# Performance work log

Hardware: AMD Instinct MI355X
Metric: run time of the kernel (lower is better)

The kernel has to match this reference:

```python
import jax, jax.numpy as jnp
import numpy as np

B, S, E, H, T = 2, 1024, 1024, 16, 32
D = E // H  # head_dim = 64
EPS = 1e-12
SCALE = float(np.sqrt(T) / np.sqrt(D))  # sqrt(num_templates) * 1/sqrt(head_dim)


def _apply_rope(q, k):
    # q, k: [B, S, H, D] float32 (source casts to float for RoPE)
    d = q.shape[-1]
    s = q.shape[1]
    inv_freq = 1.0 / (10000.0 ** (jnp.arange(0, d, 2, dtype=jnp.float32) / d))
    ang = jnp.arange(s, dtype=jnp.float32)[:, None] * inv_freq[None, :]  # [S, D/2]
    cis = jnp.exp(1j * ang)[None, :, None, :]  # [1, S, 1, D/2] complex64

    def rot(v):
        vc = v.reshape(v.shape[:-1] + (d // 2, 2))
        vc = jax.lax.complex(vc[..., 0], vc[..., 1]) * cis
        return jnp.stack([jnp.real(vc), jnp.imag(vc)], axis=-1).reshape(v.shape)

    return rot(q), rot(k)


def _l2norm(v):
    # F.normalize(v, dim=-1): v / max(||v||, eps)
    n = jnp.sqrt(jnp.sum(v * v, axis=-1, keepdims=True))
    return v / jnp.maximum(n, EPS)


def _forward(x, Wq, Wk, Wv, Wo, templates, bind_proj):
    b, s, e = x.shape
    h, d = H, D
    q = (x @ Wq.T).reshape(b, s, h, d)
    k = (x @ Wk.T).reshape(b, s, h, d)
    v = (x @ Wv.T).reshape(b, s, h, d)
    q, k = _apply_rope(q, k)
    q = q.transpose(0, 2, 1, 3)  # [B,H,S,D]
    k = k.transpose(0, 2, 1, 3)
    v = v.transpose(0, 2, 1, 3)

    tpl = _l2norm(templates)  # [H,T,D]
    # forward rfft uses norm='ortho' in the source
    q_freq = jnp.fft.rfft(q, axis=-1, norm='ortho')  # [B,H,S,F], F=D//2+1
    k_freq = jnp.fft.rfft(k, axis=-1, norm='ortho')
    t_conj = jnp.conj(jnp.fft.rfft(tpl, axis=-1, norm='ortho'))[None, :, None, :, :]  # [1,H,1,T,F]

    # NOTE: irfft in the source uses the DEFAULT 'backward' norm (asymmetric with
    # the ortho rfft) -- reproduce that exactly.
    q_bind = jnp.fft.irfft(q_freq[:, :, :, None, :] * t_conj, n=d, axis=-1)  # [B,H,S,T,D]
    k_bind = jnp.fft.irfft(k_freq[:, :, :, None, :] * t_conj, n=d, axis=-1)

    proj = bind_proj[None, :, None, None, :]  # [1,H,1,1,D]
    q_sig = _l2norm(jnp.sum(q_bind * proj, axis=-1))  # [B,H,S,T]
    k_sig = _l2norm(jnp.sum(k_bind * proj, axis=-1))

    scores = jnp.einsum('bhqt,bhkt->bhqk', q_sig, k_sig) * SCALE  # [B,H,S,S]
    attn = jax.nn.softmax(scores, axis=-1)  # dropout is identity in eval mode
    out = jnp.einsum('bhqk,bhkd->bqhd', attn, v).reshape(b, s, e)
    return out @ Wo.T


def setup_inputs() -> dict:
    key = jax.random.key(0)
    ks = jax.random.split(key, 7)
    lim = 1.0 / np.sqrt(E)
    x = jax.random.normal(ks[0], (B, S, E), jnp.float32)
    Wq = jax.random.uniform(ks[1], (E, E), jnp.float32, -lim, lim)
    Wk = jax.random.uniform(ks[2], (E, E), jnp.float32, -lim, lim)
    Wv = jax.random.uniform(ks[3], (E, E), jnp.float32, -lim, lim)
    Wo = jax.random.uniform(ks[4], (E, E), jnp.float32, -lim, lim)
    templates = jax.random.normal(ks[5], (H, T, D), jnp.float32)
    bind_proj = jax.random.normal(ks[6], (H, D), jnp.float32) * 0.02
    return {"x": x, "Wq": Wq, "Wk": Wk, "Wv": Wv, "Wo": Wo,
            "templates": templates, "bind_proj": bind_proj}


def reference(x, Wq, Wk, Wv, Wo, templates, bind_proj):
    return _forward(x, Wq, Wk, Wv, Wo, templates, bind_proj)
```

## Files before the change

kernel.cpp:

```cpp
#include <hip/hip_runtime.h>
#include <math.h>

#define S_ 1024
#define T_ 32
#define SCALE_F 0.7071067811865476f

typedef unsigned int uint;
typedef unsigned short ushort;
typedef __bf16 bf16x8 __attribute__((ext_vector_type(8)));
typedef float f32x16 __attribute__((ext_vector_type(16)));

union FragU { uint4 q; bf16x8 v; };

#define MFMA(a, b, c) __builtin_amdgcn_mfma_f32_32x32x16_bf16((a), (b), (c), 0, 0, 0)

__device__ __forceinline__ uint rne16(float f) {
  uint u = __builtin_bit_cast(uint, f);
  u += 0x7fffu + ((u >> 16) & 1u);
  return u >> 16;
}

__device__ __forceinline__ float bf2f(ushort u) {
  return __builtin_bit_cast(float, ((uint)u) << 16);
}

__device__ __forceinline__ void split8a(const float* f, uint4& hi, uint4& lo) {
  uint h[8], m[8];
#pragma unroll
  for (int i = 0; i < 8; ++i) {
    uint u = __builtin_bit_cast(uint, f[i]);
    h[i] = u >> 16;
    float fh = __builtin_bit_cast(float, u & 0xffff0000u);
    m[i] = __builtin_bit_cast(uint, f[i] - fh) >> 16;
  }
  hi = make_uint4(h[0] | (h[1] << 16), h[2] | (h[3] << 16),
                  h[4] | (h[5] << 16), h[6] | (h[7] << 16));
  lo = make_uint4(m[0] | (m[1] << 16), m[2] | (m[3] << 16),
                  m[4] | (m[5] << 16), m[6] | (m[7] << 16));
}

__device__ __forceinline__ uint4 rne8(const float4& A, const float4& B) {
  float f[8] = {A.x, A.y, A.z, A.w, B.x, B.y, B.z, B.w};
  uint h[8];
#pragma unroll
  for (int i = 0; i < 8; ++i) h[i] = rne16(f[i]);
  return make_uint4(h[0] | (h[1] << 16), h[2] | (h[3] << 16),
                    h[4] | (h[5] << 16), h[6] | (h[7] << 16));
}

__global__ __launch_bounds__(256) void k_prep(
    const float* __restrict__ X, const float* __restrict__ Wq,
    const float* __restrict__ Wk, const float* __restrict__ Wv,
    const float* __restrict__ Wo, const float* __restrict__ tpl,
    const float* __restrict__ proj, ushort* __restrict__ Xb,
    ushort* __restrict__ Wqb, ushort* __restrict__ Wkb,
    ushort* __restrict__ Wvb, ushort* __restrict__ Wob,
    float* __restrict__ cs, ushort* __restrict__ Ahh,
    ushort* __restrict__ Ahl) {
  const int bid = blockIdx.x;
  const int tid = threadIdx.x;

  if (bid < 3072) {
    int i = bid * 256 + tid;
    const float* src;
    ushort* dst;
    int j;
    if (i < 262144)      { src = X;  dst = Xb;  j = i; }
    else if (i < 393216) { src = Wq; dst = Wqb; j = i - 262144; }
    else if (i < 524288) { src = Wk; dst = Wkb; j = i - 393216; }
    else if (i < 655360) { src = Wv; dst = Wvb; j = i - 524288; }
    else                 { src = Wo; dst = Wob; j = i - 655360; }
    float4 a = *reinterpret_cast<const float4*>(src + j * 8);
    float4 b = *reinterpret_cast<const float4*>(src + j * 8 + 4);
    *reinterpret_cast<uint4*>(dst + j * 8) = rne8(a, b);
    return;
  }

  if (bid < 3200) {
    int j = (bid - 3072) * 256 + tid;
    int s = j >> 5, p = j & 31;
    float invf = powf(10000.0f, (-2.0f * p) / 64.0f);
    float sn, c;
    sincosf((float)s * invf, &sn, &c);
    cs[s * 64 + 2 * p] = c;
    cs[s * 64 + 2 * p + 1] = sn;
    return;
  }

  {
    __shared__ float tn[4][64];
    int wid = tid >> 6, lane = tid & 63;
    int ht = (bid - 3200) * 4 + wid;
    int h = ht >> 5;
    float tv = tpl[ht * 64 + lane];
    float ss = tv * tv;
#pragma unroll
    for (int off2 = 1; off2 < 64; off2 <<= 1) ss += __shfl_xor(ss, off2);
    float rn = 1.0f / fmaxf(sqrtf(ss), 1e-12f);
    tn[wid][lane] = tv * rn;
    __syncthreads();
    float acc = 0.f;
#pragma unroll
    for (int j2 = 0; j2 < 64; ++j2)
      acc += proj[h * 64 + j2] * tn[wid][(lane - j2) & 63];
    float v = acc * 0.125f;
    uint u = __builtin_bit_cast(uint, v);
    uint hi = u >> 16;
    float fh = __builtin_bit_cast(float, u & 0xffff0000u);
    uint lo = __builtin_bit_cast(uint, v - fh) >> 16;
    Ahh[ht * 64 + lane] = (ushort)hi;
    Ahl[ht * 64 + lane] = (ushort)lo;
  }
}

__global__ __launch_bounds__(256) void k_qkv(
    const ushort* __restrict__ Xb,
    const ushort* __restrict__ Wqb, const ushort* __restrict__ Wkb,
    const ushort* __restrict__ Wvb,
    const ushort* __restrict__ Ahh, const ushort* __restrict__ Ahl,
    const float* __restrict__ cs,
    ushort* __restrict__ Qs, ushort* __restrict__ Ks,
    ushort* __restrict__ Vt) {
  __shared__ __align__(16) char smem[34816];

  const int z = blockIdx.z;
  const ushort* Wm = (z == 0) ? Wqb : (z == 1) ? Wkb : Wvb;
  const int m0 = blockIdx.y * 128;
  const int n0 = blockIdx.x * 64;
  const int h = blockIdx.x;

  const int tid = threadIdx.x;
  const int l = tid & 63;
  const int wid = tid >> 6;
  const int wr = wid >> 1, wc = wid & 1;
  const int l31 = l & 31, lhi = l >> 5;

  const int sr = tid >> 2;
  const int sc = tid & 3;

  const int offA0 = (sr) * 64 + ((sc ^ ((sr >> 1) & 3)) << 4);
  const int offA1 = (sr + 64) * 64 + ((sc ^ (((sr + 64) >> 1) & 3)) << 4);
  const int offB = 8192 + sr * 64 + ((sc ^ ((sr >> 1) & 3)) << 4);

  const ushort* apsrc0 = Xb + (size_t)(m0 + sr) * 1024 + sc * 8;
  const ushort* apsrc1 = Xb + (size_t)(m0 + sr + 64) * 1024 + sc * 8;
  const ushort* bpsrc = Wm + (size_t)(n0 + sr) * 1024 + sc * 8;

  f32x16 acc0 = 0.0f, acc1 = 0.0f;

  {
    *reinterpret_cast<uint4*>(smem + offA0) =
        *reinterpret_cast<const uint4*>(apsrc0);
    *reinterpret_cast<uint4*>(smem + offA1) =
        *reinterpret_cast<const uint4*>(apsrc1);
    *reinterpret_cast<uint4*>(smem + offB) =
        *reinterpret_cast<const uint4*>(bpsrc);
  }
  uint4 ra0 = *reinterpret_cast<const uint4*>(apsrc0 + 32);
  uint4 ra1 = *reinterpret_cast<const uint4*>(apsrc1 + 32);
  uint4 rb = *reinterpret_cast<const uint4*>(bpsrc + 32);
  __syncthreads();

  int cur = 0;
#pragma unroll 4
  for (int t = 0; t < 32; ++t) {
    uint4 na0, na1, nb;
    if (t < 30) {
      const int kn = (t + 2) * 32;
      na0 = *reinterpret_cast<const uint4*>(apsrc0 + kn);
      na1 = *reinterpret_cast<const uint4*>(apsrc1 + kn);
      nb = *reinterpret_cast<const uint4*>(bpsrc + kn);
    }

    const char* base = smem + cur * 12288;
#pragma unroll
    for (int kst = 0; kst < 2; ++kst) {
      FragU ah0, ah1, bh;
      {
        int row = wr * 64 + l31;
        int cc = (kst * 2 + lhi) ^ ((row >> 1) & 3);
        ah0.q = *reinterpret_cast<const uint4*>(base + row * 64 + cc * 16);
      }
      {
        int row = wr * 64 + 32 + l31;
        int cc = (kst * 2 + lhi) ^ ((row >> 1) & 3);
        ah1.q = *reinterpret_cast<const uint4*>(base + row * 64 + cc * 16);
      }
      {
        int brow = wc * 32 + l31;
        int bcc = (kst * 2 + lhi) ^ ((brow >> 1) & 3);
        bh.q = *reinterpret_cast<const uint4*>(base + 8192 + brow * 64 + bcc * 16);
      }
      acc0 = MFMA(ah0.v, bh.v, acc0);
      acc1 = MFMA(ah1.v, bh.v, acc1);
    }

    if (t < 31) {
      char* dst = smem + (cur ^ 1) * 12288;
      *reinterpret_cast<uint4*>(dst + offA0) = ra0;
      *reinterpret_cast<uint4*>(dst + offA1) = ra1;
      *reinterpret_cast<uint4*>(dst + offB) = rb;
      __syncthreads();
      cur ^= 1;
      if (t < 30) { ra0 = na0; ra1 = na1; rb = nb; }
    }
  }

  if (z == 2) {
    int d = wc * 32 + l31;
#pragma unroll
    for (int fm = 0; fm < 2; ++fm) {
      const f32x16& a = fm ? acc1 : acc0;
#pragma unroll
      for (int j = 0; j < 16; ++j) {
        int rl = fm * 32 + (j & 3) + ((j >> 2) & 3) * 8 + 4 * lhi;
        int m = m0 + wr * 64 + rl;
        int b = m >> 10, s = m & 1023;
        Vt[((size_t)((b * 16 + h) * 64 + d)) * 1024 + s] = (ushort)rne16(a[j]);
      }
    }
    return;
  }

  ushort* Sig = (z == 0) ? Qs : Ks;
  float* dmp = reinterpret_cast<float*>(smem);
  __syncthreads();
#pragma unroll
  for (int fm = 0; fm < 2; ++fm) {
    const f32x16& a = fm ? acc1 : acc0;
#pragma unroll
    for (int j = 0; j < 16; ++j) {
      int rl = fm * 32 + (j & 3) + ((j >> 2) & 3) * 8 + 4 * lhi;
      dmp[(wr * 64 + rl) * 68 + wc * 32 + l31] = a[j];
    }
  }
  __syncthreads();

  int srow = wr * 64 + wc * 32 + l31;
  int sq = (m0 + srow) & 1023;
  f32x16 sacc = 0.0f;
#pragma unroll
  for (int kst = 0; kst < 4; ++kst) {
    const float* dp = &dmp[srow * 68 + kst * 16 + lhi * 8];
    float4 x0 = *reinterpret_cast<const float4*>(dp);
    float4 x1 = *reinterpret_cast<const float4*>(dp + 4);
    const float* cp = &cs[sq * 64 + kst * 16 + lhi * 8];
    float4 c0 = *reinterpret_cast<const float4*>(cp);
    float4 c1 = *reinterpret_cast<const float4*>(cp + 4);
    float r[8];
    r[0] = x0.x * c0.x - x0.y * c0.y;
    r[1] = x0.x * c0.y + x0.y * c0.x;
    r[2] = x0.z * c0.z - x0.w * c0.w;
    r[3] = x0.z * c0.w + x0.w * c0.z;
    r[4] = x1.x * c1.x - x1.y * c1.y;
    r[5] = x1.x * c1.y + x1.y * c1.x;
    r[6] = x1.z * c1.z - x1.w * c1.w;
    r[7] = x1.z * c1.w + x1.w * c1.z;
    FragU ah, al;
    split8a(r, ah.q, al.q);
    size_t boff = ((size_t)(h * 32 + l31) * 64 + kst * 16 + lhi * 8);
    FragU bh, bl;
    bh.q = *reinterpret_cast<const uint4*>(Ahh + boff);
    bl.q = *reinterpret_cast<const uint4*>(Ahl + boff);
    sacc = MFMA(al.v, bh.v, sacc);
    sacc = MFMA(ah.v, bl.v, sacc);
    sacc = MFMA(ah.v, bh.v, sacc);
  }
#pragma unroll
  for (int j = 0; j < 16; ++j) {
    float v = sacc[j];
    float ss = v * v;
    ss += __shfl_xor(ss, 1);
    ss += __shfl_xor(ss, 2);
    ss += __shfl_xor(ss, 4);
    ss += __shfl_xor(ss, 8);
    ss += __shfl_xor(ss, 16);
    float rn = 1.0f / fmaxf(sqrtf(ss), 1e-12f);
    int rl = (j & 3) + ((j >> 2) & 3) * 8 + 4 * lhi;
    int m = m0 + wr * 64 + wc * 32 + rl;
    int bb = m >> 10, s2 = m & 1023;
    Sig[(((size_t)(bb * 16 + h)) * 1024 + s2) * 32 + l31] =
        (ushort)rne16(v * rn);
  }
}

__global__ __launch_bounds__(128) void k_attn(const ushort* __restrict__ Qs,
                                              const ushort* __restrict__ Ks,
                                              const ushort* __restrict__ Vt,
                                              ushort* __restrict__ Po,
                                              float* __restrict__ Pd) {
  __shared__ ushort plds[2][32][68];

  const int tid = threadIdx.x;
  const int l = tid & 63;
  const int wid = tid >> 6;
  const int l31 = l & 31, lhi = l >> 5;
  const int bh = blockIdx.y;
  const int z = blockIdx.z;
  const int q0 = blockIdx.x * 64 + wid * 32;

  FragU aq0, aq1;
  {
    const ushort* qp = Qs + ((size_t)bh * 1024 + q0 + l31) * 32 + lhi * 8;
    aq0.q = *reinterpret_cast<const uint4*>(qp);
    aq1.q = *reinterpret_cast<const uint4*>(qp + 16);
  }

  const ushort* kbase = Ks + (size_t)bh * 1024 * 32;
  const ushort* vbase = Vt + (size_t)bh * 64 * 1024;

  f32x16 oacc0 = 0.0f, oacc1 = 0.0f;
  float pden[16];
#pragma unroll
  for (int r = 0; r < 16; ++r) pden[r] = 0.f;

  const int ktBeg = z * 4;
  FragU kc00, kc01, kc10, kc11;
  {
    const ushort* kp0 = kbase + (size_t)(ktBeg * 64 + l31) * 32 + lhi * 8;
    const ushort* kp1 = kbase + (size_t)(ktBeg * 64 + 32 + l31) * 32 + lhi * 8;
    kc00.q = *reinterpret_cast<const uint4*>(kp0);
    kc01.q = *reinterpret_cast<const uint4*>(kp0 + 16);
    kc10.q = *reinterpret_cast<const uint4*>(kp1);
    kc11.q = *reinterpret_cast<const uint4*>(kp1 + 16);
  }

#pragma unroll
  for (int ki = 0; ki < 4; ++ki) {
    const int kt = ktBeg + ki;
    const int k0 = kt * 64;

    FragU vv00, vv01, vv10, vv11, vv20, vv21, vv30, vv31;
    {
      const ushort* vp = vbase + (size_t)l31 * 1024 + k0 + lhi * 8;
      vv00.q = *reinterpret_cast<const uint4*>(vp);
      vv01.q = *reinterpret_cast<const uint4*>(vp + 32 * 1024);
      vv10.q = *reinterpret_cast<const uint4*>(vp + 16);
      vv11.q = *reinterpret_cast<const uint4*>(vp + 16 + 32 * 1024);
      vv20.q = *reinterpret_cast<const uint4*>(vp + 32);
      vv21.q = *reinterpret_cast<const uint4*>(vp + 32 + 32 * 1024);
      vv30.q = *reinterpret_cast<const uint4*>(vp + 48);
      vv31.q = *reinterpret_cast<const uint4*>(vp + 48 + 32 * 1024);
    }

    f32x16 sacc0 = 0.0f, sacc1 = 0.0f;
    sacc0 = MFMA(aq0.v, kc00.v, sacc0);
    sacc0 = MFMA(aq1.v, kc01.v, sacc0);
    sacc1 = MFMA(aq0.v, kc10.v, sacc1);
    sacc1 = MFMA(aq1.v, kc11.v, sacc1);

    FragU kn00, kn01, kn10, kn11;
    if (ki < 3) {
      const ushort* kp0 = kbase + (size_t)((kt + 1) * 64 + l31) * 32 + lhi * 8;
      const ushort* kp1 =
          kbase + (size_t)((kt + 1) * 64 + 32 + l31) * 32 + lhi * 8;
      kn00.q = *reinterpret_cast<const uint4*>(kp0);
      kn01.q = *reinterpret_cast<const uint4*>(kp0 + 16);
      kn10.q = *reinterpret_cast<const uint4*>(kp1);
      kn11.q = *reinterpret_cast<const uint4*>(kp1 + 16);
    }

#pragma unroll
    for (int r = 0; r < 16; ++r) {
      float e0 = __expf(sacc0[r] * SCALE_F);
      float e1 = __expf(sacc1[r] * SCALE_F);
      pden[r] += e0 + e1;
      int q = (r & 3) + ((r >> 2) << 3) + 4 * lhi;
      plds[wid][q][l31] = (ushort)rne16(e0);
      plds[wid][q][32 + l31] = (ushort)rne16(e1);
    }
    __builtin_amdgcn_wave_barrier();

#pragma unroll
    for (int kst = 0; kst < 4; ++kst) {
      FragU ap;
      const ushort* pp = &plds[wid][l31][kst * 16 + lhi * 8];
      uint2 plo = *reinterpret_cast<const uint2*>(pp);
      uint2 phi = *reinterpret_cast<const uint2*>(pp + 4);
      ap.q = make_uint4(plo.x, plo.y, phi.x, phi.y);
      const FragU& b0 = (kst == 0) ? vv00 : (kst == 1) ? vv10 : (kst == 2) ? vv20 : vv30;
      const FragU& b1 = (kst == 0) ? vv01 : (kst == 1) ? vv11 : (kst == 2) ? vv21 : vv31;
      oacc0 = MFMA(ap.v, b0.v, oacc0);
      oacc1 = MFMA(ap.v, b1.v, oacc1);
    }

    if (ki < 3) { kc00 = kn00; kc01 = kn01; kc10 = kn10; kc11 = kn11; }
  }

#pragma unroll
  for (int r = 0; r < 16; ++r) {
    float s = pden[r];
    s += __shfl_xor(s, 1);
    s += __shfl_xor(s, 2);
    s += __shfl_xor(s, 4);
    s += __shfl_xor(s, 8);
    s += __shfl_xor(s, 16);
    pden[r] = s;
  }

  const size_t zb = (size_t)z * 32 + bh;
#pragma unroll
  for (int r = 0; r < 16; ++r) {
    int q = q0 + (r & 3) + ((r >> 2) << 3) + 4 * lhi;
    size_t row = zb * 1024 + q;
    Po[row * 64 + l31] = (ushort)rne16(oacc0[r]);
    Po[row * 64 + 32 + l31] = (ushort)rne16(oacc1[r]);
    if (l31 == 0) Pd[row] = pden[r];
  }
}

__global__ __launch_bounds__(256) void k_attnred(const ushort* __restrict__ Po,
                                                 const float* __restrict__ Pd,
                                                 ushort* __restrict__ O) {
  int idx = blockIdx.x * 4 + (threadIdx.x >> 6);
  int d = threadIdx.x & 63;
  float den = 0.f, val = 0.f;
#pragma unroll
  for (int zc = 0; zc < 4; ++zc) {
    size_t row = (size_t)zc * 32768 + idx;
    den += Pd[row];
    val += bf2f(Po[row * 64 + d]);
  }
  int bh = idx >> 10, q = idx & 1023;
  int b = bh >> 4, h = bh & 15;
  O[((size_t)(b * 1024 + q)) * 1024 + h * 64 + d] = (ushort)rne16(val / den);
}

__global__ __launch_bounds__(128) void k_attn_mono(const ushort* __restrict__ Qs,
                                                   const ushort* __restrict__ Ks,
                                                   const ushort* __restrict__ Vt,
                                                   ushort* __restrict__ O) {
  __shared__ ushort plds[2][32][68];

  const int tid = threadIdx.x;
  const int l = tid & 63;
  const int wid = tid >> 6;
  const int l31 = l & 31, lhi = l >> 5;
  const int bh = blockIdx.y;
  const int q0 = blockIdx.x * 64 + wid * 32;

  FragU aq0, aq1;
  {
    const ushort* qp = Qs + ((size_t)bh * 1024 + q0 + l31) * 32 + lhi * 8;
    aq0.q = *reinterpret_cast<const uint4*>(qp);
    aq1.q = *reinterpret_cast<const uint4*>(qp + 16);
  }

  const ushort* kbase = Ks + (size_t)bh * 1024 * 32;
  const ushort* vbase = Vt + (size_t)bh * 64 * 1024;

  f32x16 oacc0 = 0.0f, oacc1 = 0.0f;
  float pden[16];
#pragma unroll
  for (int r = 0; r < 16; ++r) pden[r] = 0.f;

  for (int kt = 0; kt < 16; ++kt) {
    const int k0 = kt * 64;
    f32x16 sacc[2];
    sacc[0] = 0.0f;
    sacc[1] = 0.0f;
#pragma unroll
    for (int nt = 0; nt < 2; ++nt) {
      const ushort* kp = kbase + (size_t)(k0 + nt * 32 + l31) * 32 + lhi * 8;
      FragU b0, b1;
      b0.q = *reinterpret_cast<const uint4*>(kp);
      b1.q = *reinterpret_cast<const uint4*>(kp + 16);
      sacc[nt] = MFMA(aq0.v, b0.v, sacc[nt]);
      sacc[nt] = MFMA(aq1.v, b1.v, sacc[nt]);
    }
#pragma unroll
    for (int nt = 0; nt < 2; ++nt) {
#pragma unroll
      for (int r = 0; r < 16; ++r) {
        float e = __expf(sacc[nt][r] * SCALE_F);
        pden[r] += e;
        int q = (r & 3) + ((r >> 2) << 3) + 4 * lhi;
        plds[wid][q][nt * 32 + l31] = (ushort)rne16(e);
      }
    }
    __builtin_amdgcn_wave_barrier();
#pragma unroll
    for (int kst = 0; kst < 4; ++kst) {
      FragU ap;
      const ushort* pp = &plds[wid][l31][kst * 16 + lhi * 8];
      uint2 plo = *reinterpret_cast<const uint2*>(pp);
      uint2 phi = *reinterpret_cast<const uint2*>(pp + 4);
      ap.q = make_uint4(plo.x, plo.y, phi.x, phi.y);
      FragU bv0, bv1;
      const ushort* vp0 = vbase + (size_t)l31 * 1024 + k0 + kst * 16 + lhi * 8;
      bv0.q = *reinterpret_cast<const uint4*>(vp0);
      bv1.q = *reinterpret_cast<const uint4*>(vp0 + 32 * 1024);
      oacc0 = MFMA(ap.v, bv0.v, oacc0);
      oacc1 = MFMA(ap.v, bv1.v, oacc1);
    }
  }

#pragma unroll
  for (int r = 0; r < 16; ++r) {
    float s = pden[r];
    s += __shfl_xor(s, 1);
    s += __shfl_xor(s, 2);
    s += __shfl_xor(s, 4);
    s += __shfl_xor(s, 8);
    s += __shfl_xor(s, 16);
    pden[r] = 1.0f / s;
  }

  const int b = bh >> 4, h = bh & 15;
#pragma unroll
  for (int r = 0; r < 16; ++r) {
    int q = q0 + (r & 3) + ((r >> 2) << 3) + 4 * lhi;
    size_t row = ((size_t)b * 1024 + q) * 1024 + h * 64;
    O[row + l31] = (ushort)rne16(oacc0[r] * pden[r]);
    O[row + 32 + l31] = (ushort)rne16(oacc1[r] * pden[r]);
  }
}

__global__ __launch_bounds__(256) void k_final(const ushort* __restrict__ Xb,
                                               const ushort* __restrict__ Wb,
                                               float* __restrict__ Y) {
  __shared__ __align__(16) char smem[16384];

  const int m0 = blockIdx.y * 64;
  const int n0 = blockIdx.x * 64;
  const int tid = threadIdx.x;
  const int l = tid & 63;
  const int wid = tid >> 6;
  const int wr = wid >> 1, wc = wid & 1;
  const int l31 = l & 31, lhi = l >> 5;
  const int sr = tid >> 2;
  const int sc = tid & 3;

  const int offA = sr * 64 + ((sc ^ ((sr >> 1) & 3)) << 4);
  const int offB = 4096 + offA;
  const ushort* apsrc = Xb + (size_t)(m0 + sr) * 1024 + sc * 8;
  const ushort* bpsrc = Wb + (size_t)(n0 + sr) * 1024 + sc * 8;

  f32x16 acc = 0.0f;

  {
    *reinterpret_cast<uint4*>(smem + offA) =
        *reinterpret_cast<const uint4*>(apsrc);
    *reinterpret_cast<uint4*>(smem + offB) =
        *reinterpret_cast<const uint4*>(bpsrc);
  }
  uint4 ra = *reinterpret_cast<const uint4*>(apsrc + 32);
  uint4 rb = *reinterpret_cast<const uint4*>(bpsrc + 32);
  __syncthreads();

  int cur = 0;
#pragma unroll 4
  for (int t = 0; t < 32; ++t) {
    uint4 na, nb;
    if (t < 30) {
      const int kn = (t + 2) * 32;
      na = *reinterpret_cast<const uint4*>(apsrc + kn);
      nb = *reinterpret_cast<const uint4*>(bpsrc + kn);
    }

    const char* base = smem + cur * 8192;
#pragma unroll
    for (int kst = 0; kst < 2; ++kst) {
      FragU ah, bh;
      int row = wr * 32 + l31;
      int cc = (kst * 2 + lhi) ^ ((row >> 1) & 3);
      ah.q = *reinterpret_cast<const uint4*>(base + row * 64 + cc * 16);
      int brow = wc * 32 + l31;
      int bcc = (kst * 2 + lhi) ^ ((brow >> 1) & 3);
      bh.q = *reinterpret_cast<const uint4*>(base + 4096 + brow * 64 + bcc * 16);
      acc = MFMA(ah.v, bh.v, acc);
    }

    if (t < 31) {
      char* dst = smem + (cur ^ 1) * 8192;
      *reinterpret_cast<uint4*>(dst + offA) = ra;
      *reinterpret_cast<uint4*>(dst + offB) = rb;
      __syncthreads();
      cur ^= 1;
      if (t < 30) { ra = na; rb = nb; }
    }
  }

#pragma unroll
  for (int j = 0; j < 16; ++j) {
    int rl = (j & 3) + ((j >> 2) & 3) * 8 + 4 * lhi;
    int m = m0 + wr * 32 + rl;
    Y[(size_t)m * 1024 + n0 + wc * 32 + l31] = acc[j];
  }
}

extern "C" void kernel_launch(void* const* d_in, const int* in_sizes, int n_in,
                              void* d_out, int out_size, void* d_ws,
                              size_t ws_size, hipStream_t stream) {
  const float* x = (const float*)d_in[0];
  const float* Wq = (const float*)d_in[1];
  const float* Wk = (const float*)d_in[2];
  const float* Wv = (const float*)d_in[3];
  const float* Wo = (const float*)d_in[4];
  const float* tpl = (const float*)d_in[5];
  const float* proj = (const float*)d_in[6];
  float* out = (float*)d_out;

  char* ws = (char*)d_ws;
  size_t off = 0;
  auto alloc = [&](size_t bytes) {
    void* p = ws + off;
    off += (bytes + 255) & ~(size_t)255;
    return p;
  };

  const size_t MB = 1024 * 1024;
  bool huge = ws_size >= 64 * MB;
  bool big = ws_size >= 22 * MB;

  ushort *Xb, *Wvb, *obuf;
  float* cs;
  ushort *Ahh, *Ahl, *Wqb, *Wkb, *Wob, *qs, *ks, *vt;
  ushort* Po = nullptr;
  float* Pd = nullptr;

  if (big || huge) {
    Xb = (ushort*)alloc(4 * MB);
    cs = (float*)alloc((size_t)1024 * 64 * 4);
    Ahh = (ushort*)alloc((size_t)16 * 32 * 64 * 2);
    Ahl = (ushort*)alloc((size_t)16 * 32 * 64 * 2);
    Wqb = (ushort*)alloc(2 * MB);
    Wkb = (ushort*)alloc(2 * MB);
    Wvb = (ushort*)alloc(2 * MB);
    Wob = (ushort*)alloc(2 * MB);
    qs = (ushort*)alloc(2 * MB);
    ks = (ushort*)alloc(2 * MB);
    vt = (ushort*)alloc(4 * MB);
    if (huge) {
      Po = (ushort*)alloc(16 * MB);
      Pd = (float*)alloc((size_t)4 * 32768 * 4);
    }
    obuf = Xb;
  } else {
    cs = (float*)alloc((size_t)1024 * 64 * 4);
    Ahh = (ushort*)alloc((size_t)16 * 32 * 64 * 2);
    Ahl = (ushort*)alloc((size_t)16 * 32 * 64 * 2);
    Wqb = (ushort*)alloc(2 * MB);
    Wkb = (ushort*)alloc(2 * MB);
    Wob = (ushort*)alloc(2 * MB);
    qs = (ushort*)alloc(2 * MB);
    ks = (ushort*)alloc(2 * MB);
    vt = (ushort*)alloc(4 * MB);
    obuf = (ushort*)ws;
    Xb = (ushort*)d_out;
    Wvb = (ushort*)((char*)d_out + 4 * MB);
  }

  k_prep<<<dim3(3328), dim3(256), 0, stream>>>(x, Wq, Wk, Wv, Wo, tpl, proj,
                                               Xb, Wqb, Wkb, Wvb, Wob, cs, Ahh,
                                               Ahl);
  k_qkv<<<dim3(16, 16, 3), dim3(256), 0, stream>>>(Xb, Wqb, Wkb, Wvb, Ahh, Ahl,
                                                   cs, qs, ks, vt);
  if (huge) {
    k_attn<<<dim3(16, 32, 4), dim3(128), 0, stream>>>(qs, ks, vt, Po, Pd);
    k_attnred<<<dim3(8192), dim3(256), 0, stream>>>(Po, Pd, obuf);
  } else {
    k_attn_mono<<<dim3(16, 32), dim3(128), 0, stream>>>(qs, ks, vt, obuf);
  }
  k_final<<<dim3(16, 32), dim3(256), 0, stream>>>(obuf, Wob, out);
}
```

Before: 86.53 us.

## Fuse Q and K projections into one block sharing the X tile

Blocks with z==0 now compute both the Q and K projections, loading each X tile into shared memory once and running four MFMA accumulators against separate Wq and Wk tiles. The two signature epilogues then run one after the other in the same block, and the grid shrinks from three z-slices to two (QK fused, V separate). This halves the X traffic for Q/K and removes a block group, but the fused blocks do twice the work and hold more registers, so occupancy drops and the grid is unbalanced: 256 heavy blocks alongside 256 light V blocks.

```diff
diff --git a/kernel.cpp b/kernel.cpp
--- a/kernel.cpp
+++ b/kernel.cpp
@@ -124,7 +124,6 @@
   __shared__ __align__(16) char smem[34816];
 
   const int z = blockIdx.z;
-  const ushort* Wm = (z == 0) ? Wqb : (z == 1) ? Wkb : Wvb;
   const int m0 = blockIdx.y * 128;
   const int n0 = blockIdx.x * 64;
   const int h = blockIdx.x;
@@ -138,75 +137,219 @@
   const int sr = tid >> 2;
   const int sc = tid & 3;
 
-  const int offA0 = (sr) * 64 + ((sc ^ ((sr >> 1) & 3)) << 4);
-  const int offA1 = (sr + 64) * 64 + ((sc ^ (((sr + 64) >> 1) & 3)) << 4);
-  const int offB = 8192 + sr * 64 + ((sc ^ ((sr >> 1) & 3)) << 4);
+  const int swzA0 = (sr) * 64 + ((sc ^ ((sr >> 1) & 3)) << 4);
+  const int swzA1 = (sr + 64) * 64 + ((sc ^ (((sr + 64) >> 1) & 3)) << 4);
+  const int swzB = sr * 64 + ((sc ^ ((sr >> 1) & 3)) << 4);
 
   const ushort* apsrc0 = Xb + (size_t)(m0 + sr) * 1024 + sc * 8;
   const ushort* apsrc1 = Xb + (size_t)(m0 + sr + 64) * 1024 + sc * 8;
-  const ushort* bpsrc = Wm + (size_t)(n0 + sr) * 1024 + sc * 8;
-
-  f32x16 acc0 = 0.0f, acc1 = 0.0f;
+
+  if (z == 0) {
+    const ushort* bqsrc = Wqb + (size_t)(n0 + sr) * 1024 + sc * 8;
+    const ushort* bksrc = Wkb + (size_t)(n0 + sr) * 1024 + sc * 8;
+    const int offA0 = swzA0, offA1 = swzA1;
+    const int offBq = 8192 + swzB, offBk = 12288 + swzB;
+
+    f32x16 aq0 = 0.0f, aq1 = 0.0f, ak0 = 0.0f, ak1 = 0.0f;
+
+    {
+      *reinterpret_cast<uint4*>(smem + offA0) =
+          *reinterpret_cast<const uint4*>(apsrc0);
+      *reinterpret_cast<uint4*>(smem + offA1) =
+          *reinterpret_cast<const uint4*>(apsrc1);
+      *reinterpret_cast<uint4*>(smem + offBq) =
+          *reinterpret_cast<const uint4*>(bqsrc);
+      *reinterpret_cast<uint4*>(smem + offBk) =
+          *reinterpret_cast<const uint4*>(bksrc);
+    }
+    uint4 ra0 = *reinterpret_cast<const uint4*>(apsrc0 + 32);
+    uint4 ra1 = *reinterpret_cast<const uint4*>(apsrc1 + 32);
+    uint4 rbq = *reinterpret_cast<const uint4*>(bqsrc + 32);
+    uint4 rbk = *reinterpret_cast<const uint4*>(bksrc + 32);
+    __syncthreads();
+
+    int cur = 0;
+#pragma unroll 2
+    for (int t = 0; t < 32; ++t) {
+      uint4 na0, na1, nbq, nbk;
+      if (t < 30) {
+        const int kn = (t + 2) * 32;
+        na0 = *reinterpret_cast<const uint4*>(apsrc0 + kn);
+        na1 = *reinterpret_cast<const uint4*>(apsrc1 + kn);
+        nbq = *reinterpret_cast<const uint4*>(bqsrc + kn);
+        nbk = *reinterpret_cast<const uint4*>(bksrc + kn);
+      }
+
+      const char* base = smem + cur * 16384;
+#pragma unroll
+      for (int kst = 0; kst < 2; ++kst) {
+        FragU ah0, ah1, bhq, bhk;
+        {
+          int row = wr * 64 + l31;
+          int cc = (kst * 2 + lhi) ^ ((row >> 1) & 3);
+          ah0.q = *reinterpret_cast<const uint4*>(base + row * 64 + cc * 16);
+        }
+        {
+          int row = wr * 64 + 32 + l31;
+          int cc = (kst * 2 + lhi) ^ ((row >> 1) & 3);
+          ah1.q = *reinterpret_cast<const uint4*>(base + row * 64 + cc * 16);
+        }
+        {
+          int brow = wc * 32 + l31;
+          int bcc = (kst * 2 + lhi) ^ ((brow >> 1) & 3);
+          bhq.q = *reinterpret_cast<const uint4*>(base + 8192 + brow * 64 + bcc * 16);
+          bhk.q = *reinterpret_cast<const uint4*>(base + 12288 + brow * 64 + bcc * 16);
+        }
+        aq0 = MFMA(ah0.v, bhq.v, aq0);
+        aq1 = MFMA(ah1.v, bhq.v, aq1);
+        ak0 = MFMA(ah0.v, bhk.v, ak0);
+        ak1 = MFMA(ah1.v, bhk.v, ak1);
+      }
+
+      if (t < 31) {
+        char* dst = smem + (cur ^ 1) * 16384;
+        *reinterpret_cast<uint4*>(dst + offA0) = ra0;
+        *reinterpret_cast<uint4*>(dst + offA1) = ra1;
+        *reinterpret_cast<uint4*>(dst + offBq) = rbq;
+        *reinterpret_cast<uint4*>(dst + offBk) = rbk;
+        __syncthreads();
+        cur ^= 1;
+        if (t < 30) { ra0 = na0; ra1 = na1; rbq = nbq; rbk = nbk; }
+      }
+    }
+
+    float* dmp = reinterpret_cast<float*>(smem);
+    for (int ep = 0; ep < 2; ++ep) {
+      const f32x16& a0 = ep ? ak0 : aq0;
+      const f32x16& a1 = ep ? ak1 : aq1;
+      ushort* Sig = ep ? Ks : Qs;
+      __syncthreads();
+#pragma unroll
+      for (int fm = 0; fm < 2; ++fm) {
+        const f32x16& a = fm ? a1 : a0;
+#pragma unroll
+        for (int j = 0; j < 16; ++j) {
+          int rl = fm * 32 + (j & 3) + ((j >> 2) & 3) * 8 + 4 * lhi;
+          dmp[(wr * 64 + rl) * 68 + wc * 32 + l31] = a[j];
+        }
+      }
+      __syncthreads();
+
+      int srow = wr * 64 + wc * 32 + l31;
+      int sq = (m0 + srow) & 1023;
+      f32x16 sacc = 0.0f;
+#pragma unroll
+      for (int kst = 0; kst < 4; ++kst) {
+        const float* dp = &dmp[srow * 68 + kst * 16 + lhi * 8];
+        float4 x0 = *reinterpret_cast<const float4*>(dp);
+        float4 x1 = *reinterpret_cast<const float4*>(dp + 4);
+        const float* cp = &cs[sq * 64 + kst * 16 + lhi * 8];
+        float4 c0 = *reinterpret_cast<const float4*>(cp);
+        float4 c1 = *reinterpret_cast<const float4*>(cp + 4);
+        float r[8];
+        r[0] = x0.x * c0.x - x0.y * c0.y;
+        r[1] = x0.x * c0.y + x0.y * c0.x;
+        r[2] = x0.z * c0.z - x0.w * c0.w;
+        r[3] = x0.z * c0.w + x0.w * c0.z;
+        r[4] = x1.x * c1.x - x1.y * c1.y;
+        r[5] = x1.x * c1.y + x1.y * c1.x;
+        r[6] = x1.z * c1.z - x1.w * c1.w;
+        r[7] = x1.z * c1.w + x1.w * c1.z;
+        FragU ah, al;
+        split8a(r, ah.q, al.q);
+        size_t boff = ((size_t)(h * 32 + l31) * 64 + kst * 16 + lhi * 8);
+        FragU bh, bl;
+        bh.q = *reinterpret_cast<const uint4*>(Ahh + boff);
+        bl.q = *reinterpret_cast<const uint4*>(Ahl + boff);
+        sacc = MFMA(al.v, bh.v, sacc);
+        sacc = MFMA(ah.v, bl.v, sacc);
+        sacc = MFMA(ah.v, bh.v, sacc);
+      }
+#pragma unroll
+      for (int j = 0; j < 16; ++j) {
+        float v = sacc[j];
+        float ss = v * v;
+        ss += __shfl_xor(ss, 1);
+        ss += __shfl_xor(ss, 2);
+        ss += __shfl_xor(ss, 4);
+        ss += __shfl_xor(ss, 8);
+        ss += __shfl_xor(ss, 16);
+        float rn = 1.0f / fmaxf(sqrtf(ss), 1e-12f);
+        int rl = (j & 3) + ((j >> 2) & 3) * 8 + 4 * lhi;
+        int m = m0 + wr * 64 + wc * 32 + rl;
+        int bb = m >> 10, s2 = m & 1023;
+        Sig[(((size_t)(bb * 16 + h)) * 1024 + s2) * 32 + l31] =
+            (ushort)rne16(v * rn);
+      }
+    }
+    return;
+  }
 
   {
-    *reinterpret_cast<uint4*>(smem + offA0) =
-        *reinterpret_cast<const uint4*>(apsrc0);
-    *reinterpret_cast<uint4*>(smem + offA1) =
-        *reinterpret_cast<const uint4*>(apsrc1);
-    *reinterpret_cast<uint4*>(smem + offB) =
-        *reinterpret_cast<const uint4*>(bpsrc);
-  }
-  uint4 ra0 = *reinterpret_cast<const uint4*>(apsrc0 + 32);
-  uint4 ra1 = *reinterpret_cast<const uint4*>(apsrc1 + 32);
-  uint4 rb = *reinterpret_cast<const uint4*>(bpsrc + 32);
-  __syncthreads();
-
-  int cur = 0;
+    const int offA0 = swzA0, offA1 = swzA1;
+    const int offB = 8192 + swzB;
+    const ushort* bpsrc = Wvb + (size_t)(n0 + sr) * 1024 + sc * 8;
+
+    f32x16 acc0 = 0.0f, acc1 = 0.0f;
+
+    {
+      *reinterpret_cast<uint4*>(smem + offA0) =
+          *reinterpret_cast<const uint4*>(apsrc0);
+      *reinterpret_cast<uint4*>(smem + offA1) =
+          *reinterpret_cast<const uint4*>(apsrc1);
+      *reinterpret_cast<uint4*>(smem + offB) =
+          *reinterpret_cast<const uint4*>(bpsrc);
+    }
+    uint4 ra0 = *reinterpret_cast<const uint4*>(apsrc0 + 32);
+    uint4 ra1 = *reinterpret_cast<const uint4*>(apsrc1 + 32);
+    uint4 rb = *reinterpret_cast<const uint4*>(bpsrc + 32);
+    __syncthreads();
+
+    int cur = 0;
 #pragma unroll 4
-  for (int t = 0; t < 32; ++t) {
-    uint4 na0, na1, nb;
-    if (t < 30) {
-      const int kn = (t + 2) * 32;
-      na0 = *reinterpret_cast<const uint4*>(apsrc0 + kn);
-      na1 = *reinterpret_cast<const uint4*>(apsrc1 + kn);
-      nb = *reinterpret_cast<const uint4*>(bpsrc + kn);
-    }
-
-    const char* base = smem + cur * 12288;
-#pragma unroll
-    for (int kst = 0; kst < 2; ++kst) {
-      FragU ah0, ah1, bh;
-      {
-        int row = wr * 64 + l31;
-        int cc = (kst * 2 + lhi) ^ ((row >> 1) & 3);
-        ah0.q = *reinterpret_cast<const uint4*>(base + row * 64 + cc * 16);
-      }
-      {
-        int row = wr * 64 + 32 + l31;
-        int cc = (kst * 2 + lhi) ^ ((row >> 1) & 3);
-        ah1.q = *reinterpret_cast<const uint4*>(base + row * 64 + cc * 16);
-      }
-      {
-        int brow = wc * 32 + l31;
-        int bcc = (kst * 2 + lhi) ^ ((brow >> 1) & 3);
-        bh.q = *reinterpret_cast<const uint4*>(base + 8192 + brow * 64 + bcc * 16);
-      }
-      acc0 = MFMA(ah0.v, bh.v, acc0);
-      acc1 = MFMA(ah1.v, bh.v, acc1);
-    }
-
-    if (t < 31) {
-      char* dst = smem + (cur ^ 1) * 12288;
-      *reinterpret_cast<uint4*>(dst + offA0) = ra0;
-      *reinterpret_cast<uint4*>(dst + offA1) = ra1;
-      *reinterpret_cast<uint4*>(dst + offB) = rb;
-      __syncthreads();
-      cur ^= 1;
-      if (t < 30) { ra0 = na0; ra1 = na1; rb = nb; }
-    }
-  }
-
-  if (z == 2) {
+    for (int t = 0; t < 32; ++t) {
+      uint4 na0, na1, nb;
+      if (t < 30) {
+        const int kn = (t + 2) * 32;
+        na0 = *reinterpret_cast<const uint4*>(apsrc0 + kn);
+        na1 = *reinterpret_cast<const uint4*>(apsrc1 + kn);
+        nb = *reinterpret_cast<const uint4*>(bpsrc + kn);
+      }
+
+      const char* base = smem + cur * 12288;
+#pragma unroll
+      for (int kst = 0; kst < 2; ++kst) {
+        FragU ah0, ah1, bh;
+        {
+          int row = wr * 64 + l31;
+          int cc = (kst * 2 + lhi) ^ ((row >> 1) & 3);
+          ah0.q = *reinterpret_cast<const uint4*>(base + row * 64 + cc * 16);
+        }
+        {
+          int row = wr * 64 + 32 + l31;
+          int cc = (kst * 2 + lhi) ^ ((row >> 1) & 3);
+          ah1.q = *reinterpret_cast<const uint4*>(base + row * 64 + cc * 16);
+        }
+        {
+          int brow = wc * 32 + l31;
+          int bcc = (kst * 2 + lhi) ^ ((brow >> 1) & 3);
+          bh.q = *reinterpret_cast<const uint4*>(base + 8192 + brow * 64 + bcc * 16);
+        }
+        acc0 = MFMA(ah0.v, bh.v, acc0);
+        acc1 = MFMA(ah1.v, bh.v, acc1);
+      }
+
+      if (t < 31) {
+        char* dst = smem + (cur ^ 1) * 12288;
+        *reinterpret_cast<uint4*>(dst + offA0) = ra0;
+        *reinterpret_cast<uint4*>(dst + offA1) = ra1;
+        *reinterpret_cast<uint4*>(dst + offB) = rb;
+        __syncthreads();
+        cur ^= 1;
+        if (t < 30) { ra0 = na0; ra1 = na1; rb = nb; }
+      }
+    }
+
     int d = wc * 32 + l31;
 #pragma unroll
     for (int fm = 0; fm < 2; ++fm) {
@@ -219,68 +362,6 @@
         Vt[((size_t)((b * 16 + h) * 64 + d)) * 1024 + s] = (ushort)rne16(a[j]);
       }
     }
-    return;
-  }
-
-  ushort* Sig = (z == 0) ? Qs : Ks;
-  float* dmp = reinterpret_cast<float*>(smem);
-  __syncthreads();
-#pragma unroll
-  for (int fm = 0; fm < 2; ++fm) {
-    const f32x16& a = fm ? acc1 : acc0;
-#pragma unroll
-    for (int j = 0; j < 16; ++j) {
-      int rl = fm * 32 + (j & 3) + ((j >> 2) & 3) * 8 + 4 * lhi;
-      dmp[(wr * 64 + rl) * 68 + wc * 32 + l31] = a[j];
-    }
-  }
-  __syncthreads();
-
-  int srow = wr * 64 + wc * 32 + l31;
-  int sq = (m0 + srow) & 1023;
-  f32x16 sacc = 0.0f;
-#pragma unroll
-  for (int kst = 0; kst < 4; ++kst) {
-    const float* dp = &dmp[srow * 68 + kst * 16 + lhi * 8];
-    float4 x0 = *reinterpret_cast<const float4*>(dp);
-    float4 x1 = *reinterpret_cast<const float4*>(dp + 4);
-    const float* cp = &cs[sq * 64 + kst * 16 + lhi * 8];
-    float4 c0 = *reinterpret_cast<const float4*>(cp);
-    float4 c1 = *reinterpret_cast<const float4*>(cp + 4);
-    float r[8];
-    r[0] = x0.x * c0.x - x0.y * c0.y;
-    r[1] = x0.x * c0.y + x0.y * c0.x;
-    r[2] = x0.z * c0.z - x0.w * c0.w;
-    r[3] = x0.z * c0.w + x0.w * c0.z;
-    r[4] = x1.x * c1.x - x1.y * c1.y;
-    r[5] = x1.x * c1.y + x1.y * c1.x;
-    r[6] = x1.z * c1.z - x1.w * c1.w;
-    r[7] = x1.z * c1.w + x1.w * c1.z;
-    FragU ah, al;
-    split8a(r, ah.q, al.q);
-    size_t boff = ((size_t)(h * 32 + l31) * 64 + kst * 16 + lhi * 8);
-    FragU bh, bl;
-    bh.q = *reinterpret_cast<const uint4*>(Ahh + boff);
-    bl.q = *reinterpret_cast<const uint4*>(Ahl + boff);
-    sacc = MFMA(al.v, bh.v, sacc);
-    sacc = MFMA(ah.v, bl.v, sacc);
-    sacc = MFMA(ah.v, bh.v, sacc);
-  }
-#pragma unroll
-  for (int j = 0; j < 16; ++j) {
-    float v = sacc[j];
-    float ss = v * v;
-    ss += __shfl_xor(ss, 1);
-    ss += __shfl_xor(ss, 2);
-    ss += __shfl_xor(ss, 4);
-    ss += __shfl_xor(ss, 8);
-    ss += __shfl_xor(ss, 16);
-    float rn = 1.0f / fmaxf(sqrtf(ss), 1e-12f);
-    int rl = (j & 3) + ((j >> 2) & 3) * 8 + 4 * lhi;
-    int m = m0 + wr * 64 + wc * 32 + rl;
-    int bb = m >> 10, s2 = m & 1023;
-    Sig[(((size_t)(bb * 16 + h)) * 1024 + s2) * 32 + l31] =
-        (ushort)rne16(v * rn);
   }
 }
 
@@ -654,7 +735,7 @@
   k_prep<<<dim3(3328), dim3(256), 0, stream>>>(x, Wq, Wk, Wv, Wo, tpl, proj,
                                                Xb, Wqb, Wkb, Wvb, Wob, cs, Ahh,
                                                Ahl);
-  k_qkv<<<dim3(16, 16, 3), dim3(256), 0, stream>>>(Xb, Wqb, Wkb, Wvb, Ahh, Ahl,
+  k_qkv<<<dim3(16, 16, 2), dim3(256), 0, stream>>>(Xb, Wqb, Wkb, Wvb, Ahh, Ahl,
                                                    cs, qs, ks, vt);
   if (huge) {
     k_attn<<<dim3(16, 32, 4), dim3(128), 0, stream>>>(qs, ks, vt, Po, Pd);
```

New measurement: 101.1 us. 1.17x slower.

## Fuse split-K attention reduction into one 512-thread block via shared memory

Applied to the files above, without the earlier changes.

The split-K attention kernel and its separate global-memory reduction kernel are merged. Each block now runs 8 waves: 2 query halves times 4 key chunks. Partial outputs and denominators from three of the chunks go through LDS and are summed by the first-chunk waves, which write the normalized output directly. This drops the 16MB partial buffer round-trip and one kernel launch, and the mono fallback path is removed. In exchange it adds block-wide barriers, uses more shared memory, and leaves the reducing waves doing extra work while the other waves sit idle.

```diff
diff --git a/kernel.cpp b/kernel.cpp
--- a/kernel.cpp
+++ b/kernel.cpp
@@ -284,20 +284,24 @@
   }
 }
 
-__global__ __launch_bounds__(128) void k_attn(const ushort* __restrict__ Qs,
+__global__ __launch_bounds__(512) void k_attn(const ushort* __restrict__ Qs,
                                               const ushort* __restrict__ Ks,
                                               const ushort* __restrict__ Vt,
-                                              ushort* __restrict__ Po,
-                                              float* __restrict__ Pd) {
-  __shared__ ushort plds[2][32][68];
+                                              ushort* __restrict__ O) {
+  __shared__ __align__(16) char smem[34816];
+  ushort* pm = reinterpret_cast<ushort*>(smem);
+  float* pd = reinterpret_cast<float*>(smem + 24576);
 
   const int tid = threadIdx.x;
   const int l = tid & 63;
   const int wid = tid >> 6;
+  const int zc = wid >> 1;
+  const int qh = wid & 1;
   const int l31 = l & 31, lhi = l >> 5;
   const int bh = blockIdx.y;
-  const int z = blockIdx.z;
-  const int q0 = blockIdx.x * 64 + wid * 32;
+  const int q0 = blockIdx.x * 64 + qh * 32;
+
+  ushort* myp = reinterpret_cast<ushort*>(smem) + wid * (32 * 68);
 
   FragU aq0, aq1;
   {
@@ -314,7 +318,7 @@
 #pragma unroll
   for (int r = 0; r < 16; ++r) pden[r] = 0.f;
 
-  const int ktBeg = z * 4;
+  const int ktBeg = zc * 4;
   FragU kc00, kc01, kc10, kc11;
   {
     const ushort* kp0 = kbase + (size_t)(ktBeg * 64 + l31) * 32 + lhi * 8;
@@ -366,15 +370,15 @@
       float e1 = __expf(sacc1[r] * SCALE_F);
       pden[r] += e0 + e1;
       int q = (r & 3) + ((r >> 2) << 3) + 4 * lhi;
-      plds[wid][q][l31] = (ushort)rne16(e0);
-      plds[wid][q][32 + l31] = (ushort)rne16(e1);
+      myp[q * 68 + l31] = (ushort)rne16(e0);
+      myp[q * 68 + 32 + l31] = (ushort)rne16(e1);
     }
     __builtin_amdgcn_wave_barrier();
 
 #pragma unroll
     for (int kst = 0; kst < 4; ++kst) {
       FragU ap;
-      const ushort* pp = &plds[wid][l31][kst * 16 + lhi * 8];
+      const ushort* pp = myp + l31 * 68 + kst * 16 + lhi * 8;
       uint2 plo = *reinterpret_cast<const uint2*>(pp);
       uint2 phi = *reinterpret_cast<const uint2*>(pp + 4);
       ap.q = make_uint4(plo.x, plo.y, phi.x, phi.y);
@@ -398,121 +402,36 @@
     pden[r] = s;
   }
 
-  const size_t zb = (size_t)z * 32 + bh;
-#pragma unroll
-  for (int r = 0; r < 16; ++r) {
-    int q = q0 + (r & 3) + ((r >> 2) << 3) + 4 * lhi;
-    size_t row = zb * 1024 + q;
-    Po[row * 64 + l31] = (ushort)rne16(oacc0[r]);
-    Po[row * 64 + 32 + l31] = (ushort)rne16(oacc1[r]);
-    if (l31 == 0) Pd[row] = pden[r];
-  }
-}
-
-__global__ __launch_bounds__(256) void k_attnred(const ushort* __restrict__ Po,
-                                                 const float* __restrict__ Pd,
-                                                 ushort* __restrict__ O) {
-  int idx = blockIdx.x * 4 + (threadIdx.x >> 6);
-  int d = threadIdx.x & 63;
-  float den = 0.f, val = 0.f;
-#pragma unroll
-  for (int zc = 0; zc < 4; ++zc) {
-    size_t row = (size_t)zc * 32768 + idx;
-    den += Pd[row];
-    val += bf2f(Po[row * 64 + d]);
-  }
-  int bh = idx >> 10, q = idx & 1023;
-  int b = bh >> 4, h = bh & 15;
-  O[((size_t)(b * 1024 + q)) * 1024 + h * 64 + d] = (ushort)rne16(val / den);
-}
-
-__global__ __launch_bounds__(128) void k_attn_mono(const ushort* __restrict__ Qs,
-                                                   const ushort* __restrict__ Ks,
-                                                   const ushort* __restrict__ Vt,
-                                                   ushort* __restrict__ O) {
-  __shared__ ushort plds[2][32][68];
-
-  const int tid = threadIdx.x;
-  const int l = tid & 63;
-  const int wid = tid >> 6;
-  const int l31 = l & 31, lhi = l >> 5;
-  const int bh = blockIdx.y;
-  const int q0 = blockIdx.x * 64 + wid * 32;
-
-  FragU aq0, aq1;
-  {
-    const ushort* qp = Qs + ((size_t)bh * 1024 + q0 + l31) * 32 + lhi * 8;
-    aq0.q = *reinterpret_cast<const uint4*>(qp);
-    aq1.q = *reinterpret_cast<const uint4*>(qp + 16);
-  }
-
-  const ushort* kbase = Ks + (size_t)bh * 1024 * 32;
-  const ushort* vbase = Vt + (size_t)bh * 64 * 1024;
-
-  f32x16 oacc0 = 0.0f, oacc1 = 0.0f;
-  float pden[16];
-#pragma unroll
-  for (int r = 0; r < 16; ++r) pden[r] = 0.f;
-
-  for (int kt = 0; kt < 16; ++kt) {
-    const int k0 = kt * 64;
-    f32x16 sacc[2];
-    sacc[0] = 0.0f;
-    sacc[1] = 0.0f;
-#pragma unroll
-    for (int nt = 0; nt < 2; ++nt) {
-      const ushort* kp = kbase + (size_t)(k0 + nt * 32 + l31) * 32 + lhi * 8;
-      FragU b0, b1;
-      b0.q = *reinterpret_cast<const uint4*>(kp);
-      b1.q = *reinterpret_cast<const uint4*>(kp + 16);
-      sacc[nt] = MFMA(aq0.v, b0.v, sacc[nt]);
-      sacc[nt] = MFMA(aq1.v, b1.v, sacc[nt]);
-    }
-#pragma unroll
-    for (int nt = 0; nt < 2; ++nt) {
-#pragma unroll
-      for (int r = 0; r < 16; ++r) {
-        float e = __expf(sacc[nt][r] * SCALE_F);
-        pden[r] += e;
-        int q = (r & 3) + ((r >> 2) << 3) + 4 * lhi;
-        plds[wid][q][nt * 32 + l31] = (ushort)rne16(e);
+  __syncthreads();
+  if (zc > 0) {
+    const int mi = (zc - 1) * 2 + qh;
+#pragma unroll
+    for (int r = 0; r < 16; ++r) {
+      int q = (r & 3) + ((r >> 2) << 3) + 4 * lhi;
+      pm[(mi * 32 + q) * 64 + l31] = (ushort)rne16(oacc0[r]);
+      pm[(mi * 32 + q) * 64 + 32 + l31] = (ushort)rne16(oacc1[r]);
+      if (l31 == 0) pd[mi * 32 + q] = pden[r];
+    }
+  }
+  __syncthreads();
+  if (zc == 0) {
+    const int b = bh >> 4, h = bh & 15;
+#pragma unroll
+    for (int r = 0; r < 16; ++r) {
+      int q = (r & 3) + ((r >> 2) << 3) + 4 * lhi;
+      float v0 = oacc0[r], v1 = oacc1[r], den = pden[r];
+#pragma unroll
+      for (int zz = 0; zz < 3; ++zz) {
+        int mi = zz * 2 + qh;
+        v0 += bf2f(pm[(mi * 32 + q) * 64 + l31]);
+        v1 += bf2f(pm[(mi * 32 + q) * 64 + 32 + l31]);
+        den += pd[mi * 32 + q];
       }
-    }
-    __builtin_amdgcn_wave_barrier();
-#pragma unroll
-    for (int kst = 0; kst < 4; ++kst) {
-      FragU ap;
-      const ushort* pp = &plds[wid][l31][kst * 16 + lhi * 8];
-      uint2 plo = *reinterpret_cast<const uint2*>(pp);
-      uint2 phi = *reinterpret_cast<const uint2*>(pp + 4);
-      ap.q = make_uint4(plo.x, plo.y, phi.x, phi.y);
-      FragU bv0, bv1;
-      const ushort* vp0 = vbase + (size_t)l31 * 1024 + k0 + kst * 16 + lhi * 8;
-      bv0.q = *reinterpret_cast<const uint4*>(vp0);
-      bv1.q = *reinterpret_cast<const uint4*>(vp0 + 32 * 1024);
-      oacc0 = MFMA(ap.v, bv0.v, oacc0);
-      oacc1 = MFMA(ap.v, bv1.v, oacc1);
-    }
-  }
-
-#pragma unroll
-  for (int r = 0; r < 16; ++r) {
-    float s = pden[r];
-    s += __shfl_xor(s, 1);
-    s += __shfl_xor(s, 2);
-    s += __shfl_xor(s, 4);
-    s += __shfl_xor(s, 8);
-    s += __shfl_xor(s, 16);
-    pden[r] = 1.0f / s;
-  }
-
-  const int b = bh >> 4, h = bh & 15;
-#pragma unroll
-  for (int r = 0; r < 16; ++r) {
-    int q = q0 + (r & 3) + ((r >> 2) << 3) + 4 * lhi;
-    size_t row = ((size_t)b * 1024 + q) * 1024 + h * 64;
-    O[row + l31] = (ushort)rne16(oacc0[r] * pden[r]);
-    O[row + 32 + l31] = (ushort)rne16(oacc1[r] * pden[r]);
+      float rden = 1.0f / den;
+      size_t row = ((size_t)(b * 1024 + q0 + q)) * 1024 + h * 64;
+      O[row + l31] = (ushort)rne16(v0 * rden);
+      O[row + 32 + l31] = (ushort)rne16(v1 * rden);
+    }
   }
 }
 
@@ -610,16 +529,13 @@
   };
 
   const size_t MB = 1024 * 1024;
-  bool huge = ws_size >= 64 * MB;
   bool big = ws_size >= 22 * MB;
 
   ushort *Xb, *Wvb, *obuf;
   float* cs;
   ushort *Ahh, *Ahl, *Wqb, *Wkb, *Wob, *qs, *ks, *vt;
-  ushort* Po = nullptr;
-  float* Pd = nullptr;
-
-  if (big || huge) {
+
+  if (big) {
     Xb = (ushort*)alloc(4 * MB);
     cs = (float*)alloc((size_t)1024 * 64 * 4);
     Ahh = (ushort*)alloc((size_t)16 * 32 * 64 * 2);
@@ -631,10 +547,6 @@
     qs = (ushort*)alloc(2 * MB);
     ks = (ushort*)alloc(2 * MB);
     vt = (ushort*)alloc(4 * MB);
-    if (huge) {
-      Po = (ushort*)alloc(16 * MB);
-      Pd = (float*)alloc((size_t)4 * 32768 * 4);
-    }
     obuf = Xb;
   } else {
     cs = (float*)alloc((size_t)1024 * 64 * 4);
@@ -656,11 +568,6 @@
                                                Ahl);
   k_qkv<<<dim3(16, 16, 3), dim3(256), 0, stream>>>(Xb, Wqb, Wkb, Wvb, Ahh, Ahl,
                                                    cs, qs, ks, vt);
-  if (huge) {
-    k_attn<<<dim3(16, 32, 4), dim3(128), 0, stream>>>(qs, ks, vt, Po, Pd);
-    k_attnred<<<dim3(8192), dim3(256), 0, stream>>>(Po, Pd, obuf);
-  } else {
-    k_attn_mono<<<dim3(16, 32), dim3(128), 0, stream>>>(qs, ks, vt, obuf);
-  }
+  k_attn<<<dim3(16, 32), dim3(512), 0, stream>>>(qs, ks, vt, obuf);
   k_final<<<dim3(16, 32), dim3(256), 0, stream>>>(obuf, Wob, out);
 }
```

New measurement: 83.85 us, median of 3. -3.1%, faster.
